# Kernel optimization log

Hardware: AMD Instinct MI355X
Metric: run time of the kernel (lower is better)

## Reference

```python
import jax, jax.numpy as jnp
import numpy as np

B, W, F = 64, 128, 64          # batch, window (node feat dim), n_features (nodes)
H, OUTW = 4, 128               # num_heads, out window size
NEG_SLOPE = 0.2                # LeakyReLU negative slope (alpha)


def setup_inputs() -> dict:
    key = jax.random.key(0)
    ks = jax.random.split(key, 6)
    scale_in = 1.0 / np.sqrt(W)
    scale_a = 1.0 / np.sqrt(OUTW)
    return {
        "x": jax.random.normal(ks[0], (B, W, F), dtype=jnp.float32),
        "W_src": jax.random.normal(ks[1], (H * OUTW, W), dtype=jnp.float32) * scale_in,
        "b_src": jnp.zeros((H * OUTW,), dtype=jnp.float32),
        "W_dst": jax.random.normal(ks[2], (H * OUTW, W), dtype=jnp.float32) * scale_in,
        "b_dst": jnp.zeros((H * OUTW,), dtype=jnp.float32),
        "attn": jax.random.normal(ks[3], (H, OUTW), dtype=jnp.float32) * scale_a,
    }


def reference(x, W_src, b_src, W_dst, b_dst, attn):
    # x: [B, W, F] -> node features nf: [B, F, W] (F nodes, W-dim features)
    nf = jnp.transpose(x, (0, 2, 1))
    b, f, w = nf.shape
    h, outw = attn.shape
    # GATv2 separate source/destination projections (share_weights=False)
    fs = (nf @ W_src.T + b_src).reshape(b, f, h, outw)  # [B, F, H, outW]
    fd = (nf @ W_dst.T + b_dst).reshape(b, f, h, outw)
    # additive score over complete graph with self-loops: e[b,i,j,h,d]
    s = fs[:, :, None, :, :] + fd[:, None, :, :, :]      # [B, src, dst, H, outW]
    e = jnp.where(s >= 0, s, NEG_SLOPE * s)              # LeakyReLU
    scores = jnp.einsum('bijhd,hd->bhij', e, attn)       # [B, H, src, dst]
    # edge softmax: normalize over incoming edges (sources) per destination
    a = jax.nn.softmax(scores, axis=2)
    # weighted scatter-sum aggregation at destinations
    out = jnp.einsum('bhij,bihd->bjhd', a, fs)           # [B, F, H, outW]
    out = out.mean(axis=2)                               # mean over heads -> [B, F, outW]
    return jnp.transpose(out, (0, 2, 1))                 # [B, outW, F]
```

## Files before the change

kernel.cpp:

```cpp
#include <hip/hip_runtime.h>
#include <math.h>

#define BB 64
#define WW 128
#define FF 64
#define HH 4
#define OW 128

__global__ __launch_bounds__(256) void gat_proj(
    const float* __restrict__ x,
    const float* __restrict__ Wsrc,
    const float* __restrict__ bsrc,
    const float* __restrict__ Wdst,
    const float* __restrict__ bdst,
    float* __restrict__ fs,
    float* __restrict__ fd)
{
    __shared__ float xl[WW * FF];
    __shared__ float wl[64 * 132];
    __shared__ float bl[64];

    const int b  = blockIdx.x >> 4;
    const int rt = blockIdx.x & 15;
    const bool is_src = rt < 8;
    const int rm0 = (rt & 7) * 64;

    const float* Wm = is_src ? Wsrc : Wdst;
    const float* bm = is_src ? bsrc : bdst;

    const int t = threadIdx.x;

    {
        const float4* xs = (const float4*)(x + (size_t)b * (WW * FF));
        float4* xd = (float4*)xl;
        #pragma unroll
        for (int p = 0; p < 8; ++p)
            xd[p * 256 + t] = xs[p * 256 + t];

        const float4* ws = (const float4*)(Wm + (size_t)rm0 * WW);
        float4* wd = (float4*)wl;
        #pragma unroll
        for (int p = 0; p < 8; ++p) {
            int idx = p * 256 + t;
            int r = idx >> 5, kq = idx & 31;
            wd[r * 33 + kq] = ws[idx];
        }
        if (t < 64) bl[t] = bm[rm0 + t];
    }
    __syncthreads();

    const int f0 = (t & 15) * 4;
    const int r0 = (t >> 4) * 4;

    float acc[4][4] = {};
    #pragma unroll
    for (int k0 = 0; k0 < WW; k0 += 4) {
        float4 xv[4], wv[4];
        #pragma unroll
        for (int kk = 0; kk < 4; ++kk)
            xv[kk] = *(const float4*)&xl[(k0 + kk) * FF + f0];
        #pragma unroll
        for (int rr = 0; rr < 4; ++rr)
            wv[rr] = *(const float4*)&wl[(r0 + rr) * 132 + k0];
        #pragma unroll
        for (int kk = 0; kk < 4; ++kk) {
            #pragma unroll
            for (int rr = 0; rr < 4; ++rr) {
                const float wf = ((const float*)&wv[rr])[kk];
                const float* xf = (const float*)&xv[kk];
                acc[rr][0] = fmaf(xf[0], wf, acc[rr][0]);
                acc[rr][1] = fmaf(xf[1], wf, acc[rr][1]);
                acc[rr][2] = fmaf(xf[2], wf, acc[rr][2]);
                acc[rr][3] = fmaf(xf[3], wf, acc[rr][3]);
            }
        }
    }

    const int h  = (rt & 7) >> 1;
    const int d0 = ((rt & 1) * 64) + r0;
    float* dst = (is_src ? fs : fd) + (((size_t)b * HH + h) * FF) * OW;
    float b0 = bl[r0 + 0], b1 = bl[r0 + 1], b2 = bl[r0 + 2], b3 = bl[r0 + 3];
    #pragma unroll
    for (int ff = 0; ff < 4; ++ff) {
        float4 o;
        o.x = acc[0][ff] + b0;
        o.y = acc[1][ff] + b1;
        o.z = acc[2][ff] + b2;
        o.w = acc[3][ff] + b3;
        *(float4*)&dst[(size_t)(f0 + ff) * OW + d0] = o;
    }
}

__global__ __launch_bounds__(256) void gat_attn(
    const float* __restrict__ fs,
    const float* __restrict__ fd,
    const float* __restrict__ attn,
    float* __restrict__ ws2)
{
    __shared__ float fsl[FF * 132];
    __shared__ float fdl[16 * OW];
    __shared__ float St[FF * 20];
    __shared__ float A6[OW], B4[OW];
    __shared__ float redm[16][16];
    __shared__ float reds[16][16];
    __shared__ float invl[16];

    const int bx = blockIdx.x;
    const int jq = bx & 3;
    const int h  = (bx >> 2) & 3;
    const int b  = bx >> 4;
    const size_t bh = (size_t)b * HH + h;
    const int jbase = jq * 16;

    const int t    = threadIdx.x;
    const int wv   = t >> 6;
    const int lane = t & 63;

    {
        const float4* s = (const float4*)(fs + bh * (FF * OW));
        float4* d4 = (float4*)fsl;
        #pragma unroll
        for (int p = 0; p < 8; ++p) {
            int idx = p * 256 + t;
            int i = idx >> 5, kq = idx & 31;
            d4[i * 33 + kq] = s[idx];
        }
        const float4* fsrc = (const float4*)(fd + (bh * FF + jbase) * OW);
        float4* fdst = (float4*)fdl;
        fdst[t]       = fsrc[t];
        fdst[t + 256] = fsrc[t + 256];
        if (t < 128) {
            float a = attn[h * OW + t];
            A6[t] = 0.6f * a;
            B4[t] = 0.4f * a;
        }
    }
    __syncthreads();

    const int jl0 = wv * 4;
    {
        float sc[4] = {0.0f, 0.0f, 0.0f, 0.0f};
        #pragma unroll
        for (int c = 0; c < 32; ++c) {
            const int d0 = c * 4;
            float4 fsv = *(const float4*)&fsl[lane * 132 + d0];
            float4 a6  = *(const float4*)&A6[d0];
            float4 b4  = *(const float4*)&B4[d0];
            #pragma unroll
            for (int jj = 0; jj < 4; ++jj) {
                float4 fdv = *(const float4*)&fdl[(jl0 + jj) * OW + d0];
                float s, r = sc[jj];
                s = fsv.x + fdv.x; r = fmaf(a6.x, s, fmaf(b4.x, fabsf(s), r));
                s = fsv.y + fdv.y; r = fmaf(a6.y, s, fmaf(b4.y, fabsf(s), r));
                s = fsv.z + fdv.z; r = fmaf(a6.z, s, fmaf(b4.z, fabsf(s), r));
                s = fsv.w + fdv.w; r = fmaf(a6.w, s, fmaf(b4.w, fabsf(s), r));
                sc[jj] = r;
            }
        }
        float4 o = {sc[0], sc[1], sc[2], sc[3]};
        *(float4*)&St[lane * 20 + jl0] = o;
    }
    __syncthreads();

    {
        const int j = t & 15, st = t >> 4;
        const int i0 = st * 4;
        float m0 = St[(i0 + 0) * 20 + j];
        float m1 = St[(i0 + 1) * 20 + j];
        float m2 = St[(i0 + 2) * 20 + j];
        float m3 = St[(i0 + 3) * 20 + j];
        redm[st][j] = fmaxf(fmaxf(m0, m1), fmaxf(m2, m3));
    }
    __syncthreads();
    {
        const int j = t & 15, st = t >> 4;
        const int i0 = st * 4;
        float mj = redm[0][j];
        #pragma unroll
        for (int s2 = 1; s2 < 16; ++s2) mj = fmaxf(mj, redm[s2][j]);
        float e0 = __expf(St[(i0 + 0) * 20 + j] - mj);
        float e1 = __expf(St[(i0 + 1) * 20 + j] - mj);
        float e2 = __expf(St[(i0 + 2) * 20 + j] - mj);
        float e3 = __expf(St[(i0 + 3) * 20 + j] - mj);
        St[(i0 + 0) * 20 + j] = e0;
        St[(i0 + 1) * 20 + j] = e1;
        St[(i0 + 2) * 20 + j] = e2;
        St[(i0 + 3) * 20 + j] = e3;
        reds[st][j] = e0 + e1 + e2 + e3;
    }
    __syncthreads();
    if (t < 16) {
        float l = 0.0f;
        #pragma unroll
        for (int s2 = 0; s2 < 16; ++s2) l += reds[s2][t];
        invl[t] = 0.25f / l;
    }
    __syncthreads();

    {
        const int j0 = (t & 3) * 4;
        const int d0 = (t >> 2) * 2;
        float ag[4][2] = {};
        #pragma unroll
        for (int i = 0; i < FF; ++i) {
            float4 pv = *(const float4*)&St[i * 20 + j0];
            float2 fv = *(const float2*)&fsl[i * 132 + d0];
            const float* pf = (const float*)&pv;
            #pragma unroll
            for (int jj = 0; jj < 4; ++jj) {
                ag[jj][0] = fmaf(pf[jj], fv.x, ag[jj][0]);
                ag[jj][1] = fmaf(pf[jj], fv.y, ag[jj][1]);
            }
        }
        float* wout = ws2 + (bh * FF + jbase) * OW;
        #pragma unroll
        for (int jj = 0; jj < 4; ++jj) {
            float ivv = invl[j0 + jj];
            float2 o = {ag[jj][0] * ivv, ag[jj][1] * ivv};
            *(float2*)&wout[(size_t)(j0 + jj) * OW + d0] = o;
        }
    }
}

__global__ __launch_bounds__(256) void gat_reduce(
    const float* __restrict__ ws2,
    float* __restrict__ out)
{
    __shared__ float tl[16][132];
    const int b  = blockIdx.x >> 2;
    const int jg = blockIdx.x & 3;
    const int t  = threadIdx.x;

    const float* base = ws2 + ((size_t)b * HH * FF + jg * 16) * OW;
    #pragma unroll
    for (int p = 0; p < 2; ++p) {
        int idx = p * 256 + t;
        int j = idx >> 5, q = idx & 31;
        const float* src = base + (size_t)j * OW + q * 4;
        float4 s0 = *(const float4*)(src);
        float4 s1 = *(const float4*)(src + (size_t)FF * OW);
        float4 s2 = *(const float4*)(src + (size_t)2 * FF * OW);
        float4 s3 = *(const float4*)(src + (size_t)3 * FF * OW);
        float4 o;
        o.x = s0.x + s1.x + s2.x + s3.x;
        o.y = s0.y + s1.y + s2.y + s3.y;
        o.z = s0.z + s1.z + s2.z + s3.z;
        o.w = s0.w + s1.w + s2.w + s3.w;
        *(float4*)&tl[j][q * 4] = o;
    }
    __syncthreads();
    #pragma unroll
    for (int it = 0; it < 8; ++it) {
        int idx = it * 256 + t;
        int j = idx & 15, d = idx >> 4;
        out[((size_t)b * OW + d) * FF + jg * 16 + j] = tl[j][d];
    }
}

extern "C" void kernel_launch(void* const* d_in, const int* in_sizes, int n_in,
                              void* d_out, int out_size, void* d_ws, size_t ws_size,
                              hipStream_t stream) {
    const float* x    = (const float*)d_in[0];
    const float* Wsrc = (const float*)d_in[1];
    const float* bsrc = (const float*)d_in[2];
    const float* Wdst = (const float*)d_in[3];
    const float* bdst = (const float*)d_in[4];
    const float* attn = (const float*)d_in[5];
    float* out = (float*)d_out;

    const size_t SL = (size_t)BB * HH * FF * OW;
    float* fs  = (float*)d_ws;
    float* fd  = fs + SL;
    float* ws2 = fd + SL;

    gat_proj  <<<BB * 16,     256, 0, stream>>>(x, Wsrc, bsrc, Wdst, bdst, fs, fd);
    gat_attn  <<<BB * HH * 4, 256, 0, stream>>>(fs, fd, attn, ws2);
    gat_reduce<<<BB * 4,      256, 0, stream>>>(ws2, out);
}
```

Measured before the change: 117.6 us.

## Factor linear LeakyReLU term out of score loop and enlarge attention tiles

The LeakyReLU score is split into a linear part (0.6*a·(fs+fd)), computed once per source and destination node as rank-1 terms, plus a 0.4*a·|fs+fd| part that stays in the pairwise loop. This removes one FMA per element of the dominant O(F²·D) score computation. Each attention block now handles 32 destinations instead of 16, halving the grid and the redundant fs loads, with the aggregation re-tiled to 16 outputs per thread. The projection kernel also stages K in two halves to cut shared memory and raise occupancy, at the cost of an extra barrier and slight rounding differences.

```diff
diff --git a/kernel.cpp b/kernel.cpp
--- a/kernel.cpp
+++ b/kernel.cpp
@@ -16,8 +16,8 @@
     float* __restrict__ fs,
     float* __restrict__ fd)
 {
-    __shared__ float xl[WW * FF];
-    __shared__ float wl[64 * 132];
+    __shared__ float xl[64 * FF];
+    __shared__ float wl[64 * 68];
     __shared__ float bl[64];
 
     const int b  = blockIdx.x >> 4;
@@ -28,52 +28,54 @@
     const float* Wm = is_src ? Wsrc : Wdst;
     const float* bm = is_src ? bsrc : bdst;
 
-    const int t = threadIdx.x;
-
-    {
-        const float4* xs = (const float4*)(x + (size_t)b * (WW * FF));
-        float4* xd = (float4*)xl;
-        #pragma unroll
-        for (int p = 0; p < 8; ++p)
-            xd[p * 256 + t] = xs[p * 256 + t];
-
-        const float4* ws = (const float4*)(Wm + (size_t)rm0 * WW);
-        float4* wd = (float4*)wl;
-        #pragma unroll
-        for (int p = 0; p < 8; ++p) {
-            int idx = p * 256 + t;
-            int r = idx >> 5, kq = idx & 31;
-            wd[r * 33 + kq] = ws[idx];
-        }
-        if (t < 64) bl[t] = bm[rm0 + t];
-    }
-    __syncthreads();
-
+    const int t  = threadIdx.x;
     const int f0 = (t & 15) * 4;
     const int r0 = (t >> 4) * 4;
 
     float acc[4][4] = {};
-    #pragma unroll
-    for (int k0 = 0; k0 < WW; k0 += 4) {
-        float4 xv[4], wv[4];
-        #pragma unroll
-        for (int kk = 0; kk < 4; ++kk)
-            xv[kk] = *(const float4*)&xl[(k0 + kk) * FF + f0];
-        #pragma unroll
-        for (int rr = 0; rr < 4; ++rr)
-            wv[rr] = *(const float4*)&wl[(r0 + rr) * 132 + k0];
-        #pragma unroll
-        for (int kk = 0; kk < 4; ++kk) {
-            #pragma unroll
-            for (int rr = 0; rr < 4; ++rr) {
-                const float wf = ((const float*)&wv[rr])[kk];
-                const float* xf = (const float*)&xv[kk];
-                acc[rr][0] = fmaf(xf[0], wf, acc[rr][0]);
-                acc[rr][1] = fmaf(xf[1], wf, acc[rr][1]);
-                acc[rr][2] = fmaf(xf[2], wf, acc[rr][2]);
-                acc[rr][3] = fmaf(xf[3], wf, acc[rr][3]);
+
+    for (int kp = 0; kp < 2; ++kp) {
+        {
+            const float4* xs = (const float4*)(x + (size_t)b * (WW * FF) + kp * 64 * FF);
+            float4* xd = (float4*)xl;
+            #pragma unroll
+            for (int p = 0; p < 4; ++p)
+                xd[p * 256 + t] = xs[p * 256 + t];
+            float4* wd = (float4*)wl;
+            #pragma unroll
+            for (int p = 0; p < 4; ++p) {
+                int idx = p * 256 + t;
+                int r = idx >> 4, kq = idx & 15;
+                wd[r * 17 + kq] =
+                    *(const float4*)(Wm + (size_t)(rm0 + r) * WW + kp * 64 + kq * 4);
             }
-        }
+            if (kp == 0 && t < 64) bl[t] = bm[rm0 + t];
+        }
+        __syncthreads();
+
+        #pragma unroll
+        for (int k0 = 0; k0 < 64; k0 += 4) {
+            float4 xv[4], wv[4];
+            #pragma unroll
+            for (int kk = 0; kk < 4; ++kk)
+                xv[kk] = *(const float4*)&xl[(k0 + kk) * FF + f0];
+            #pragma unroll
+            for (int rr = 0; rr < 4; ++rr)
+                wv[rr] = *(const float4*)&wl[(r0 + rr) * 68 + k0];
+            #pragma unroll
+            for (int kk = 0; kk < 4; ++kk) {
+                #pragma unroll
+                for (int rr = 0; rr < 4; ++rr) {
+                    const float wf = ((const float*)&wv[rr])[kk];
+                    const float* xf = (const float*)&xv[kk];
+                    acc[rr][0] = fmaf(xf[0], wf, acc[rr][0]);
+                    acc[rr][1] = fmaf(xf[1], wf, acc[rr][1]);
+                    acc[rr][2] = fmaf(xf[2], wf, acc[rr][2]);
+                    acc[rr][3] = fmaf(xf[3], wf, acc[rr][3]);
+                }
+            }
+        }
+        __syncthreads();
     }
 
     const int h  = (rt & 7) >> 1;
@@ -98,19 +100,20 @@
     float* __restrict__ ws2)
 {
     __shared__ float fsl[FF * 132];
-    __shared__ float fdl[16 * OW];
-    __shared__ float St[FF * 20];
+    __shared__ float fdl[32 * 132];
+    __shared__ float St[FF * 36];
     __shared__ float A6[OW], B4[OW];
-    __shared__ float redm[16][16];
-    __shared__ float reds[16][16];
-    __shared__ float invl[16];
+    __shared__ float cs[FF], cd[32];
+    __shared__ float redm[8][32];
+    __shared__ float reds[8][32];
+    __shared__ float invl[32];
 
     const int bx = blockIdx.x;
-    const int jq = bx & 3;
-    const int h  = (bx >> 2) & 3;
-    const int b  = bx >> 4;
+    const int jh = bx & 1;
+    const int h  = (bx >> 1) & 3;
+    const int b  = bx >> 3;
     const size_t bh = (size_t)b * HH + h;
-    const int jbase = jq * 16;
+    const int jbase = jh * 32;
 
     const int t    = threadIdx.x;
     const int wv   = t >> 6;
@@ -127,8 +130,12 @@
         }
         const float4* fsrc = (const float4*)(fd + (bh * FF + jbase) * OW);
         float4* fdst = (float4*)fdl;
-        fdst[t]       = fsrc[t];
-        fdst[t + 256] = fsrc[t + 256];
+        #pragma unroll
+        for (int p = 0; p < 4; ++p) {
+            int idx = p * 256 + t;
+            int j = idx >> 5, kq = idx & 31;
+            fdst[j * 33 + kq] = fsrc[idx];
+        }
         if (t < 128) {
             float a = attn[h * OW + t];
             A6[t] = 0.6f * a;
@@ -137,87 +144,125 @@
     }
     __syncthreads();
 
-    const int jl0 = wv * 4;
-    {
-        float sc[4] = {0.0f, 0.0f, 0.0f, 0.0f};
-        #pragma unroll
+    if (t < 64) {
+        float s = 0.0f;
+        #pragma unroll 8
+        for (int c = 0; c < 32; ++c) {
+            float4 fv = *(const float4*)&fsl[t * 132 + c * 4];
+            float4 av = *(const float4*)&A6[c * 4];
+            s = fmaf(fv.x, av.x, fmaf(fv.y, av.y, fmaf(fv.z, av.z, fmaf(fv.w, av.w, s))));
+        }
+        cs[t] = s;
+    } else if (t < 96) {
+        const int j = t - 64;
+        float s = 0.0f;
+        #pragma unroll 8
+        for (int c = 0; c < 32; ++c) {
+            float4 fv = *(const float4*)&fdl[j * 132 + c * 4];
+            float4 av = *(const float4*)&A6[c * 4];
+            s = fmaf(fv.x, av.x, fmaf(fv.y, av.y, fmaf(fv.z, av.z, fmaf(fv.w, av.w, s))));
+        }
+        cd[j] = s;
+    }
+    __syncthreads();
+
+    const int jl0 = wv * 8;
+    {
+        float sc[8] = {};
+        #pragma unroll 4
         for (int c = 0; c < 32; ++c) {
             const int d0 = c * 4;
             float4 fsv = *(const float4*)&fsl[lane * 132 + d0];
-            float4 a6  = *(const float4*)&A6[d0];
             float4 b4  = *(const float4*)&B4[d0];
             #pragma unroll
-            for (int jj = 0; jj < 4; ++jj) {
-                float4 fdv = *(const float4*)&fdl[(jl0 + jj) * OW + d0];
-                float s, r = sc[jj];
-                s = fsv.x + fdv.x; r = fmaf(a6.x, s, fmaf(b4.x, fabsf(s), r));
-                s = fsv.y + fdv.y; r = fmaf(a6.y, s, fmaf(b4.y, fabsf(s), r));
-                s = fsv.z + fdv.z; r = fmaf(a6.z, s, fmaf(b4.z, fabsf(s), r));
-                s = fsv.w + fdv.w; r = fmaf(a6.w, s, fmaf(b4.w, fabsf(s), r));
+            for (int jj = 0; jj < 8; ++jj) {
+                float4 fdv = *(const float4*)&fdl[(jl0 + jj) * 132 + d0];
+                float r = sc[jj];
+                r = fmaf(b4.x, fabsf(fsv.x + fdv.x), r);
+                r = fmaf(b4.y, fabsf(fsv.y + fdv.y), r);
+                r = fmaf(b4.z, fabsf(fsv.z + fdv.z), r);
+                r = fmaf(b4.w, fabsf(fsv.w + fdv.w), r);
                 sc[jj] = r;
             }
         }
-        float4 o = {sc[0], sc[1], sc[2], sc[3]};
-        *(float4*)&St[lane * 20 + jl0] = o;
-    }
-    __syncthreads();
-
-    {
-        const int j = t & 15, st = t >> 4;
-        const int i0 = st * 4;
-        float m0 = St[(i0 + 0) * 20 + j];
-        float m1 = St[(i0 + 1) * 20 + j];
-        float m2 = St[(i0 + 2) * 20 + j];
-        float m3 = St[(i0 + 3) * 20 + j];
-        redm[st][j] = fmaxf(fmaxf(m0, m1), fmaxf(m2, m3));
-    }
-    __syncthreads();
-    {
-        const int j = t & 15, st = t >> 4;
-        const int i0 = st * 4;
+        const float csl = cs[lane];
+        float4 o0, o1;
+        o0.x = sc[0] + csl + cd[jl0 + 0];
+        o0.y = sc[1] + csl + cd[jl0 + 1];
+        o0.z = sc[2] + csl + cd[jl0 + 2];
+        o0.w = sc[3] + csl + cd[jl0 + 3];
+        o1.x = sc[4] + csl + cd[jl0 + 4];
+        o1.y = sc[5] + csl + cd[jl0 + 5];
+        o1.z = sc[6] + csl + cd[jl0 + 6];
+        o1.w = sc[7] + csl + cd[jl0 + 7];
+        *(float4*)&St[lane * 36 + jl0]     = o0;
+        *(float4*)&St[lane * 36 + jl0 + 4] = o1;
+    }
+    __syncthreads();
+
+    {
+        const int j = t & 31, st = t >> 5;
+        const int i0 = st * 8;
+        float m = St[i0 * 36 + j];
+        #pragma unroll
+        for (int k = 1; k < 8; ++k) m = fmaxf(m, St[(i0 + k) * 36 + j]);
+        redm[st][j] = m;
+    }
+    __syncthreads();
+    {
+        const int j = t & 31, st = t >> 5;
+        const int i0 = st * 8;
         float mj = redm[0][j];
         #pragma unroll
-        for (int s2 = 1; s2 < 16; ++s2) mj = fmaxf(mj, redm[s2][j]);
-        float e0 = __expf(St[(i0 + 0) * 20 + j] - mj);
-        float e1 = __expf(St[(i0 + 1) * 20 + j] - mj);
-        float e2 = __expf(St[(i0 + 2) * 20 + j] - mj);
-        float e3 = __expf(St[(i0 + 3) * 20 + j] - mj);
-        St[(i0 + 0) * 20 + j] = e0;
-        St[(i0 + 1) * 20 + j] = e1;
-        St[(i0 + 2) * 20 + j] = e2;
-        St[(i0 + 3) * 20 + j] = e3;
-        reds[st][j] = e0 + e1 + e2 + e3;
-    }
-    __syncthreads();
-    if (t < 16) {
+        for (int s2 = 1; s2 < 8; ++s2) mj = fmaxf(mj, redm[s2][j]);
+        float ps = 0.0f;
+        #pragma unroll
+        for (int k = 0; k < 8; ++k) {
+            float e = __expf(St[(i0 + k) * 36 + j] - mj);
+            St[(i0 + k) * 36 + j] = e;
+            ps += e;
+        }
+        reds[st][j] = ps;
+    }
+    __syncthreads();
+    if (t < 32) {
         float l = 0.0f;
         #pragma unroll
-        for (int s2 = 0; s2 < 16; ++s2) l += reds[s2][t];
+        for (int s2 = 0; s2 < 8; ++s2) l += reds[s2][t];
         invl[t] = 0.25f / l;
     }
     __syncthreads();
 
     {
-        const int j0 = (t & 3) * 4;
-        const int d0 = (t >> 2) * 2;
-        float ag[4][2] = {};
-        #pragma unroll
+        const int dg = t & 7;
+        const int jr = t >> 3;
+        float ag[16] = {};
         for (int i = 0; i < FF; ++i) {
-            float4 pv = *(const float4*)&St[i * 20 + j0];
-            float2 fv = *(const float2*)&fsl[i * 132 + d0];
-            const float* pf = (const float*)&pv;
-            #pragma unroll
-            for (int jj = 0; jj < 4; ++jj) {
-                ag[jj][0] = fmaf(pf[jj], fv.x, ag[jj][0]);
-                ag[jj][1] = fmaf(pf[jj], fv.y, ag[jj][1]);
-            }
-        }
-        float* wout = ws2 + (bh * FF + jbase) * OW;
-        #pragma unroll
-        for (int jj = 0; jj < 4; ++jj) {
-            float ivv = invl[j0 + jj];
-            float2 o = {ag[jj][0] * ivv, ag[jj][1] * ivv};
-            *(float2*)&wout[(size_t)(j0 + jj) * OW + d0] = o;
+            const float p = St[i * 36 + jr];
+            const float* fr = &fsl[i * 132 + dg * 4];
+            float4 f0 = *(const float4*)(fr);
+            float4 f1 = *(const float4*)(fr + 32);
+            float4 f2 = *(const float4*)(fr + 64);
+            float4 f3 = *(const float4*)(fr + 96);
+            ag[0]  = fmaf(p, f0.x, ag[0]);  ag[1]  = fmaf(p, f0.y, ag[1]);
+            ag[2]  = fmaf(p, f0.z, ag[2]);  ag[3]  = fmaf(p, f0.w, ag[3]);
+            ag[4]  = fmaf(p, f1.x, ag[4]);  ag[5]  = fmaf(p, f1.y, ag[5]);
+            ag[6]  = fmaf(p, f1.z, ag[6]);  ag[7]  = fmaf(p, f1.w, ag[7]);
+            ag[8]  = fmaf(p, f2.x, ag[8]);  ag[9]  = fmaf(p, f2.y, ag[9]);
+            ag[10] = fmaf(p, f2.z, ag[10]); ag[11] = fmaf(p, f2.w, ag[11]);
+            ag[12] = fmaf(p, f3.x, ag[12]); ag[13] = fmaf(p, f3.y, ag[13]);
+            ag[14] = fmaf(p, f3.z, ag[14]); ag[15] = fmaf(p, f3.w, ag[15]);
+        }
+        const float iv = invl[jr];
+        float* wout = ws2 + (bh * FF + jbase + jr) * OW + dg * 4;
+        #pragma unroll
+        for (int q = 0; q < 4; ++q) {
+            float4 o;
+            o.x = ag[q * 4 + 0] * iv;
+            o.y = ag[q * 4 + 1] * iv;
+            o.z = ag[q * 4 + 2] * iv;
+            o.w = ag[q * 4 + 3] * iv;
+            *(float4*)&wout[q * 32] = o;
         }
     }
 }
@@ -274,6 +319,6 @@
     float* ws2 = fd + SL;
 
     gat_proj  <<<BB * 16,     256, 0, stream>>>(x, Wsrc, bsrc, Wdst, bdst, fs, fd);
-    gat_attn  <<<BB * HH * 4, 256, 0, stream>>>(fs, fd, attn, ws2);
+    gat_attn  <<<BB * HH * 2, 256, 0, stream>>>(fs, fd, attn, ws2);
     gat_reduce<<<BB * 4,      256, 0, stream>>>(ws2, out);
 }
```

New measurement: 115.5 us. Within noise of the previous version (-1.8%).

## Retile projection over batch pairs and restructure attention with linear-term factoring

Applied to the files above, without the earlier changes.

The projection kernel now processes two batch items per block with 128 threads and an 8x8 register tile, staging x and a transposed weight slice in two K-halves. The attention kernel handles all 64 destinations per (batch, head) block and splits LeakyReLU as 0.6*a·(fs+fd) + 0.4*a·|fs+fd|. The linear part becomes per-node dot products precomputed once, so the pairwise loop only evaluates the abs term. Score and aggregation loops use 4x4 and 4x8 register tiles. This aims to cut redundant fs loads and pairwise arithmetic, at the cost of fewer blocks (256 attention blocks, 512 projection blocks) and larger shared memory per block.

```diff
diff --git a/kernel.cpp b/kernel.cpp
--- a/kernel.cpp
+++ b/kernel.cpp
@@ -7,7 +7,7 @@
 #define HH 4
 #define OW 128
 
-__global__ __launch_bounds__(256) void gat_proj(
+__global__ __launch_bounds__(128) void gat_proj(
     const float* __restrict__ x,
     const float* __restrict__ Wsrc,
     const float* __restrict__ bsrc,
@@ -16,78 +16,94 @@
     float* __restrict__ fs,
     float* __restrict__ fd)
 {
-    __shared__ float xl[WW * FF];
-    __shared__ float wl[64 * 132];
+    __shared__ float x2l[64 * 132];
+    __shared__ float wlt[64 * 68];
     __shared__ float bl[64];
 
-    const int b  = blockIdx.x >> 4;
+    const int bp = blockIdx.x >> 4;
     const int rt = blockIdx.x & 15;
     const bool is_src = rt < 8;
     const int rm0 = (rt & 7) * 64;
+    const int b0  = bp * 2;
 
     const float* Wm = is_src ? Wsrc : Wdst;
     const float* bm = is_src ? bsrc : bdst;
 
-    const int t = threadIdx.x;
-
-    {
-        const float4* xs = (const float4*)(x + (size_t)b * (WW * FF));
-        float4* xd = (float4*)xl;
-        #pragma unroll
-        for (int p = 0; p < 8; ++p)
-            xd[p * 256 + t] = xs[p * 256 + t];
-
-        const float4* ws = (const float4*)(Wm + (size_t)rm0 * WW);
-        float4* wd = (float4*)wl;
+    const int t  = threadIdx.x;
+    const int tx = t & 15;
+    const int ty = t >> 4;
+
+    float acc[8][8] = {};
+
+    for (int kp = 0; kp < 2; ++kp) {
+        #pragma unroll
+        for (int p = 0; p < 16; ++p) {
+            int idx = p * 128 + t;
+            int k = idx >> 5, fq = idx & 31;
+            int bb = fq >> 4, fi = fq & 15;
+            float4 v = *(const float4*)(x + (((size_t)(b0 + bb) * WW) + kp * 64 + k) * FF + fi * 4);
+            *(float4*)&x2l[k * 132 + bb * 64 + fi * 4] = v;
+        }
         #pragma unroll
         for (int p = 0; p < 8; ++p) {
-            int idx = p * 256 + t;
-            int r = idx >> 5, kq = idx & 31;
-            wd[r * 33 + kq] = ws[idx];
-        }
-        if (t < 64) bl[t] = bm[rm0 + t];
-    }
-    __syncthreads();
-
-    const int f0 = (t & 15) * 4;
-    const int r0 = (t >> 4) * 4;
-
-    float acc[4][4] = {};
+            int idx = p * 128 + t;
+            int r = idx >> 4, kq = idx & 15;
+            float4 v = *(const float4*)(Wm + (size_t)(rm0 + r) * WW + kp * 64 + kq * 4);
+            wlt[(kq * 4 + 0) * 68 + r] = v.x;
+            wlt[(kq * 4 + 1) * 68 + r] = v.y;
+            wlt[(kq * 4 + 2) * 68 + r] = v.z;
+            wlt[(kq * 4 + 3) * 68 + r] = v.w;
+        }
+        if (kp == 0 && t < 64) bl[t] = bm[rm0 + t];
+        __syncthreads();
+
+        #pragma unroll 8
+        for (int k = 0; k < 64; ++k) {
+            const float* xa = &x2l[k * 132 + tx * 4];
+            float4 xv0 = *(const float4*)xa;
+            float4 xv1 = *(const float4*)(xa + 64);
+            const float* wa = &wlt[k * 68 + ty * 8];
+            float4 wv0 = *(const float4*)wa;
+            float4 wv1 = *(const float4*)(wa + 4);
+            const float* xf0 = (const float*)&xv0;
+            const float* xf1 = (const float*)&xv1;
+            const float* wf0 = (const float*)&wv0;
+            const float* wf1 = (const float*)&wv1;
+            #pragma unroll
+            for (int rr = 0; rr < 4; ++rr) {
+                const float w0 = wf0[rr], w1 = wf1[rr];
+                #pragma unroll
+                for (int e = 0; e < 4; ++e) {
+                    acc[rr][e]         = fmaf(w0, xf0[e], acc[rr][e]);
+                    acc[rr][4 + e]     = fmaf(w0, xf1[e], acc[rr][4 + e]);
+                    acc[4 + rr][e]     = fmaf(w1, xf0[e], acc[4 + rr][e]);
+                    acc[4 + rr][4 + e] = fmaf(w1, xf1[e], acc[4 + rr][4 + e]);
+                }
+            }
+        }
+        __syncthreads();
+    }
+
+    const int h  = rm0 >> 7;
+    const int d0 = (rm0 & 127) + ty * 8;
+    float* base = (is_src ? fs : fd);
     #pragma unroll
-    for (int k0 = 0; k0 < WW; k0 += 4) {
-        float4 xv[4], wv[4];
-        #pragma unroll
-        for (int kk = 0; kk < 4; ++kk)
-            xv[kk] = *(const float4*)&xl[(k0 + kk) * FF + f0];
-        #pragma unroll
-        for (int rr = 0; rr < 4; ++rr)
-            wv[rr] = *(const float4*)&wl[(r0 + rr) * 132 + k0];
-        #pragma unroll
-        for (int kk = 0; kk < 4; ++kk) {
-            #pragma unroll
-            for (int rr = 0; rr < 4; ++rr) {
-                const float wf = ((const float*)&wv[rr])[kk];
-                const float* xf = (const float*)&xv[kk];
-                acc[rr][0] = fmaf(xf[0], wf, acc[rr][0]);
-                acc[rr][1] = fmaf(xf[1], wf, acc[rr][1]);
-                acc[rr][2] = fmaf(xf[2], wf, acc[rr][2]);
-                acc[rr][3] = fmaf(xf[3], wf, acc[rr][3]);
-            }
-        }
-    }
-
-    const int h  = (rt & 7) >> 1;
-    const int d0 = ((rt & 1) * 64) + r0;
-    float* dst = (is_src ? fs : fd) + (((size_t)b * HH + h) * FF) * OW;
-    float b0 = bl[r0 + 0], b1 = bl[r0 + 1], b2 = bl[r0 + 2], b3 = bl[r0 + 3];
-    #pragma unroll
-    for (int ff = 0; ff < 4; ++ff) {
-        float4 o;
-        o.x = acc[0][ff] + b0;
-        o.y = acc[1][ff] + b1;
-        o.z = acc[2][ff] + b2;
-        o.w = acc[3][ff] + b3;
-        *(float4*)&dst[(size_t)(f0 + ff) * OW + d0] = o;
+    for (int bb = 0; bb < 2; ++bb) {
+        #pragma unroll
+        for (int e = 0; e < 4; ++e) {
+            const int i = tx * 4 + e;
+            const int col = bb * 4 + e;
+            float* dst = base + ((((size_t)(b0 + bb) * HH + h) * FF) + i) * OW + d0;
+            #pragma unroll
+            for (int q = 0; q < 2; ++q) {
+                float4 o;
+                o.x = acc[q * 4 + 0][col] + bl[ty * 8 + q * 4 + 0];
+                o.y = acc[q * 4 + 1][col] + bl[ty * 8 + q * 4 + 1];
+                o.z = acc[q * 4 + 2][col] + bl[ty * 8 + q * 4 + 2];
+                o.w = acc[q * 4 + 3][col] + bl[ty * 8 + q * 4 + 3];
+                *(float4*)&dst[q * 4] = o;
+            }
+        }
     }
 }
 
@@ -98,19 +114,17 @@
     float* __restrict__ ws2)
 {
     __shared__ float fsl[FF * 132];
-    __shared__ float fdl[16 * OW];
-    __shared__ float St[FF * 20];
+    __shared__ float fdt[OW * 68];
+    __shared__ float St[FF * 68];
     __shared__ float A6[OW], B4[OW];
-    __shared__ float redm[16][16];
-    __shared__ float reds[16][16];
-    __shared__ float invl[16];
-
-    const int bx = blockIdx.x;
-    const int jq = bx & 3;
-    const int h  = (bx >> 2) & 3;
-    const int b  = bx >> 4;
+    __shared__ float cs[FF], cd[FF];
+    __shared__ float redm[4][FF];
+    __shared__ float reds[4][FF];
+    __shared__ float invl[FF];
+
+    const int h = blockIdx.x & 3;
+    const int b = blockIdx.x >> 2;
     const size_t bh = (size_t)b * HH + h;
-    const int jbase = jq * 16;
 
     const int t    = threadIdx.x;
     const int wv   = t >> 6;
@@ -118,17 +132,23 @@
 
     {
         const float4* s = (const float4*)(fs + bh * (FF * OW));
-        float4* d4 = (float4*)fsl;
         #pragma unroll
         for (int p = 0; p < 8; ++p) {
             int idx = p * 256 + t;
             int i = idx >> 5, kq = idx & 31;
-            d4[i * 33 + kq] = s[idx];
-        }
-        const float4* fsrc = (const float4*)(fd + (bh * FF + jbase) * OW);
-        float4* fdst = (float4*)fdl;
-        fdst[t]       = fsrc[t];
-        fdst[t + 256] = fsrc[t + 256];
+            *(float4*)&fsl[i * 132 + kq * 4] = s[idx];
+        }
+        const float* fdg = fd + bh * (FF * OW);
+        #pragma unroll
+        for (int p = 0; p < 8; ++p) {
+            int dq = p * 4 + wv;
+            int j  = lane;
+            float4 v = *(const float4*)(fdg + (size_t)j * OW + dq * 4);
+            fdt[(dq * 4 + 0) * 68 + j] = v.x;
+            fdt[(dq * 4 + 1) * 68 + j] = v.y;
+            fdt[(dq * 4 + 2) * 68 + j] = v.z;
+            fdt[(dq * 4 + 3) * 68 + j] = v.w;
+        }
         if (t < 128) {
             float a = attn[h * OW + t];
             A6[t] = 0.6f * a;
@@ -137,87 +157,130 @@
     }
     __syncthreads();
 
-    const int jl0 = wv * 4;
-    {
-        float sc[4] = {0.0f, 0.0f, 0.0f, 0.0f};
-        #pragma unroll
+    if (wv == 0) {
+        float s = 0.0f;
+        #pragma unroll 8
+        for (int c = 0; c < 32; ++c) {
+            float4 fv = *(const float4*)&fsl[lane * 132 + c * 4];
+            float4 av = *(const float4*)&A6[c * 4];
+            s = fmaf(fv.x, av.x, fmaf(fv.y, av.y, fmaf(fv.z, av.z, fmaf(fv.w, av.w, s))));
+        }
+        cs[lane] = s;
+    } else if (wv == 1) {
+        float s = 0.0f;
+        #pragma unroll 16
+        for (int d = 0; d < OW; ++d)
+            s = fmaf(fdt[d * 68 + lane], A6[d], s);
+        cd[lane] = s;
+    }
+    __syncthreads();
+
+    {
+        const int ig = t >> 4, jg = t & 15;
+        const int i0 = ig * 4, j0 = jg * 4;
+        float sc[4][4] = {};
+        #pragma unroll 2
         for (int c = 0; c < 32; ++c) {
             const int d0 = c * 4;
-            float4 fsv = *(const float4*)&fsl[lane * 132 + d0];
-            float4 a6  = *(const float4*)&A6[d0];
-            float4 b4  = *(const float4*)&B4[d0];
-            #pragma unroll
-            for (int jj = 0; jj < 4; ++jj) {
-                float4 fdv = *(const float4*)&fdl[(jl0 + jj) * OW + d0];
-                float s, r = sc[jj];
-                s = fsv.x + fdv.x; r = fmaf(a6.x, s, fmaf(b4.x, fabsf(s), r));
-                s = fsv.y + fdv.y; r = fmaf(a6.y, s, fmaf(b4.y, fabsf(s), r));
-                s = fsv.z + fdv.z; r = fmaf(a6.z, s, fmaf(b4.z, fabsf(s), r));
-                s = fsv.w + fdv.w; r = fmaf(a6.w, s, fmaf(b4.w, fabsf(s), r));
-                sc[jj] = r;
-            }
-        }
-        float4 o = {sc[0], sc[1], sc[2], sc[3]};
-        *(float4*)&St[lane * 20 + jl0] = o;
-    }
-    __syncthreads();
-
-    {
-        const int j = t & 15, st = t >> 4;
-        const int i0 = st * 4;
-        float m0 = St[(i0 + 0) * 20 + j];
-        float m1 = St[(i0 + 1) * 20 + j];
-        float m2 = St[(i0 + 2) * 20 + j];
-        float m3 = St[(i0 + 3) * 20 + j];
-        redm[st][j] = fmaxf(fmaxf(m0, m1), fmaxf(m2, m3));
-    }
-    __syncthreads();
-    {
-        const int j = t & 15, st = t >> 4;
-        const int i0 = st * 4;
-        float mj = redm[0][j];
-        #pragma unroll
-        for (int s2 = 1; s2 < 16; ++s2) mj = fmaxf(mj, redm[s2][j]);
-        float e0 = __expf(St[(i0 + 0) * 20 + j] - mj);
-        float e1 = __expf(St[(i0 + 1) * 20 + j] - mj);
-        float e2 = __expf(St[(i0 + 2) * 20 + j] - mj);
-        float e3 = __expf(St[(i0 + 3) * 20 + j] - mj);
-        St[(i0 + 0) * 20 + j] = e0;
-        St[(i0 + 1) * 20 + j] = e1;
-        St[(i0 + 2) * 20 + j] = e2;
-        St[(i0 + 3) * 20 + j] = e3;
-        reds[st][j] = e0 + e1 + e2 + e3;
-    }
-    __syncthreads();
-    if (t < 16) {
-        float l = 0.0f;
-        #pragma unroll
-        for (int s2 = 0; s2 < 16; ++s2) l += reds[s2][t];
-        invl[t] = 0.25f / l;
-    }
-    __syncthreads();
-
-    {
-        const int j0 = (t & 3) * 4;
-        const int d0 = (t >> 2) * 2;
-        float ag[4][2] = {};
-        #pragma unroll
+            float4 fsv[4], fdv[4];
+            #pragma unroll
+            for (int m = 0; m < 4; ++m)
+                fsv[m] = *(const float4*)&fsl[(i0 + m) * 132 + d0];
+            #pragma unroll
+            for (int e = 0; e < 4; ++e)
+                fdv[e] = *(const float4*)&fdt[(d0 + e) * 68 + j0];
+            float4 b4 = *(const float4*)&B4[d0];
+            const float* bf = (const float*)&b4;
+            #pragma unroll
+            for (int m = 0; m < 4; ++m) {
+                const float* fm = (const float*)&fsv[m];
+                #pragma unroll
+                for (int e = 0; e < 4; ++e) {
+                    const float* fe = (const float*)&fdv[e];
+                    const float fv = fm[e], be = bf[e];
+                    sc[m][0] = fmaf(be, fabsf(fv + fe[0]), sc[m][0]);
+                    sc[m][1] = fmaf(be, fabsf(fv + fe[1]), sc[m][1]);
+                    sc[m][2] = fmaf(be, fabsf(fv + fe[2]), sc[m][2]);
+                    sc[m][3] = fmaf(be, fabsf(fv + fe[3]), sc[m][3]);
+                }
+            }
+        }
+        float4 cdv = *(const float4*)&cd[j0];
+        #pragma unroll
+        for (int m = 0; m < 4; ++m) {
+            const float csm = cs[i0 + m];
+            float4 o;
+            o.x = sc[m][0] + csm + cdv.x;
+            o.y = sc[m][1] + csm + cdv.y;
+            o.z = sc[m][2] + csm + cdv.z;
+            o.w = sc[m][3] + csm + cdv.w;
+            *(float4*)&St[(i0 + m) * 68 + j0] = o;
+        }
+    }
+    __syncthreads();
+
+    {
+        const int st = t >> 6, j = t & 63;
+        const int i0 = st * 16;
+        float m = St[i0 * 68 + j];
+        #pragma unroll
+        for (int ii = 1; ii < 16; ++ii) m = fmaxf(m, St[(i0 + ii) * 68 + j]);
+        redm[st][j] = m;
+    }
+    __syncthreads();
+    {
+        const int st = t >> 6, j = t & 63;
+        const int i0 = st * 16;
+        float mj = fmaxf(fmaxf(redm[0][j], redm[1][j]), fmaxf(redm[2][j], redm[3][j]));
+        float ps = 0.0f;
+        #pragma unroll
+        for (int ii = 0; ii < 16; ++ii) {
+            float e = __expf(St[(i0 + ii) * 68 + j] - mj);
+            St[(i0 + ii) * 68 + j] = e;
+            ps += e;
+        }
+        reds[st][j] = ps;
+    }
+    __syncthreads();
+    if (t < 64)
+        invl[t] = 0.25f / (reds[0][t] + reds[1][t] + reds[2][t] + reds[3][t]);
+    __syncthreads();
+
+    {
+        const int jg = t & 15, dg = t >> 4;
+        const int j0 = jg * 4, d0 = dg * 8;
+        float ag[4][8] = {};
+        #pragma unroll 2
         for (int i = 0; i < FF; ++i) {
-            float4 pv = *(const float4*)&St[i * 20 + j0];
-            float2 fv = *(const float2*)&fsl[i * 132 + d0];
+            float4 pv = *(const float4*)&St[i * 68 + j0];
+            float4 f0 = *(const float4*)&fsl[i * 132 + d0];
+            float4 f1 = *(const float4*)&fsl[i * 132 + d0 + 4];
             const float* pf = (const float*)&pv;
-            #pragma unroll
-            for (int jj = 0; jj < 4; ++jj) {
-                ag[jj][0] = fmaf(pf[jj], fv.x, ag[jj][0]);
-                ag[jj][1] = fmaf(pf[jj], fv.y, ag[jj][1]);
-            }
-        }
-        float* wout = ws2 + (bh * FF + jbase) * OW;
-        #pragma unroll
-        for (int jj = 0; jj < 4; ++jj) {
-            float ivv = invl[j0 + jj];
-            float2 o = {ag[jj][0] * ivv, ag[jj][1] * ivv};
-            *(float2*)&wout[(size_t)(j0 + jj) * OW + d0] = o;
+            const float* fa = (const float*)&f0;
+            const float* fb = (const float*)&f1;
+            #pragma unroll
+            for (int n = 0; n < 4; ++n) {
+                const float p = pf[n];
+                #pragma unroll
+                for (int e = 0; e < 4; ++e) {
+                    ag[n][e]     = fmaf(p, fa[e], ag[n][e]);
+                    ag[n][4 + e] = fmaf(p, fb[e], ag[n][4 + e]);
+                }
+            }
+        }
+        float* wout = ws2 + (bh * FF) * OW;
+        #pragma unroll
+        for (int n = 0; n < 4; ++n) {
+            const float iv = invl[j0 + n];
+            #pragma unroll
+            for (int q = 0; q < 2; ++q) {
+                float4 o;
+                o.x = ag[n][q * 4 + 0] * iv;
+                o.y = ag[n][q * 4 + 1] * iv;
+                o.z = ag[n][q * 4 + 2] * iv;
+                o.w = ag[n][q * 4 + 3] * iv;
+                *(float4*)&wout[(size_t)(j0 + n) * OW + d0 + q * 4] = o;
+            }
         }
     }
 }
@@ -273,7 +336,7 @@
     float* fd  = fs + SL;
     float* ws2 = fd + SL;
 
-    gat_proj  <<<BB * 16,     256, 0, stream>>>(x, Wsrc, bsrc, Wdst, bdst, fs, fd);
-    gat_attn  <<<BB * HH * 4, 256, 0, stream>>>(fs, fd, attn, ws2);
-    gat_reduce<<<BB * 4,      256, 0, stream>>>(ws2, out);
+    gat_proj  <<<32 * 16, 128, 0, stream>>>(x, Wsrc, bsrc, Wdst, bdst, fs, fd);
+    gat_attn  <<<BB * HH, 256, 0, stream>>>(fs, fd, attn, ws2);
+    gat_reduce<<<BB * 4,  256, 0, stream>>>(ws2, out);
 }
```

After: 121.2 us. 1.03x slower.
